# Kernel optimization log

Measured on AMD Instinct MI355X. Metric: run time of the kernel, lower is better.

The kernel has to match this reference:

```python
import jax, jax.numpy as jnp
import numpy as np

# hps: rnn_size=512, num_mixture=5, input_seq_width=35, output_seq_width=32,
#      batch_size=128, max_seq_len=1000
B, T, D_IN, Z, H, K = 128, 1000, 35, 32, 512, 5
OUT = 3 * K * Z  # 3 * num_mixture * output_seq_width = 480


def setup_inputs() -> dict:
    key = jax.random.key(0)
    ks = jax.random.split(key, 5)
    scale = 0.05
    return {
        "inputs": jax.random.normal(ks[0], (B, T, D_IN), jnp.float32),
        # Keras LSTMCell params: kernel [D,4H], recurrent_kernel [H,4H], bias [4H]
        # gate order: i, f, g(candidate), o
        "Wk": jax.random.normal(ks[1], (D_IN, 4 * H), jnp.float32) * scale,
        "Wr": jax.random.normal(ks[2], (H, 4 * H), jnp.float32) * scale,
        "b": jnp.zeros((4 * H,), jnp.float32),
        # MDN Dense head: [H, 3*K*Z]
        "Wd": jax.random.normal(ks[3], (H, OUT), jnp.float32) * scale,
        "bd": jnp.zeros((OUT,), jnp.float32),
    }


def reference(inputs, Wk, Wr, b, Wd, bd):
    # split into (vae_z, a) then concat back -> identity, kept for faithfulness
    vae_z, a = inputs[..., :Z], inputs[..., Z:]
    z_a = jnp.concatenate([vae_z, a], axis=2)  # [B, T, D_IN]

    # precompute input projection for all timesteps (hoisted out of the scan)
    xz = jnp.einsum('btd,dk->btk', z_a, Wk) + b  # [B, T, 4H]
    xz_t = jnp.swapaxes(xz, 0, 1)                # [T, B, 4H]

    h0 = jnp.zeros((z_a.shape[0], H), xz.dtype)

    def step(carry, xt):
        h, c = carry
        gates = xt + h @ Wr  # [B, 4H]
        i, f, g, o = jnp.split(gates, 4, axis=-1)
        c = jax.nn.sigmoid(f) * c + jax.nn.sigmoid(i) * jnp.tanh(g)
        h = jax.nn.sigmoid(o) * jnp.tanh(c)
        return (h, c), h

    _, hs = jax.lax.scan(step, (h0, h0), xz_t)   # hs: [T, B, H]
    rnn_out = jnp.swapaxes(hs, 0, 1).reshape(-1, H)  # [B*T, H]
    out = rnn_out @ Wd + bd  # [B*T, 3*K*Z] mu/logstd/logpi MDN params
    return out
```

## Files before the change

### kernel.cpp

```cpp
#include <hip/hip_runtime.h>


#define NGRP   8
#define NSLICE 32
#define GB     16
#define HH     512
#define TT     1000
#define DIN    35
#define OUTC   480
#define ODC    15
#define HWORDS 2048

typedef __bf16 bf16x8 __attribute__((ext_vector_type(8)));
typedef float  f32x4  __attribute__((ext_vector_type(4)));
typedef unsigned short u16;
typedef unsigned int   u32;
typedef unsigned long long u64;

__device__ __forceinline__ u16 f2bf(float x) {
    u32 u = __float_as_uint(x);
    u += 0x7FFFu + ((u >> 16) & 1u);
    return (u16)(u >> 16);
}
__device__ __forceinline__ float sigf(float x) { return 1.0f / (1.0f + __expf(-x)); }
__device__ __forceinline__ float tanh_fast(float x) {
    float ax = fabsf(x);
    float e = __expf(-2.0f * ax);
    return copysignf((1.0f - e) / (1.0f + e), x);
}
__device__ __forceinline__ u32 pk2f(float a, float b) {
    return (u32)f2bf(a) | ((u32)f2bf(b) << 16);
}

union bf8u { u32 u[4]; bf16x8 v; };

#define BARRIER() do { asm volatile("" ::: "memory"); \
                       __builtin_amdgcn_s_barrier(); \
                       asm volatile("" ::: "memory"); \
                       __builtin_amdgcn_sched_barrier(0); } while (0)
#define WAIT_LGKM() do { asm volatile("s_waitcnt lgkmcnt(0)" ::: "memory"); \
                         __builtin_amdgcn_sched_barrier(0); } while (0)
#define WAIT_VM()   do { asm volatile("s_waitcnt vmcnt(0)" ::: "memory"); \
                         __builtin_amdgcn_sched_barrier(0); } while (0)

#define MFMA16(a, b, c) __builtin_amdgcn_mfma_f32_16x16x32_bf16((a), (b), (c), 0, 0, 0)

__global__ void __launch_bounds__(512, 1)
mdn_kernel(const float* __restrict__ inp, const float* __restrict__ Wk,
           const float* __restrict__ Wr,  const float* __restrict__ bg,
           const float* __restrict__ Wd,  const float* __restrict__ bd,
           float* __restrict__ out, u32* __restrict__ flags, u64* __restrict__ hbuf)
{
    __shared__ __attribute__((aligned(16))) u16  wr_s[64 * HH];
    __shared__ __attribute__((aligned(16))) u16  wk_s[64 * 64];
    __shared__ __attribute__((aligned(16))) u16  wd_s[16 * HH];
    __shared__ __attribute__((aligned(16))) u16  h_s [GB * HH];
    __shared__ __attribute__((aligned(16))) float gbuf[4 * 256];
    __shared__ __attribute__((aligned(16))) float pbuf[2 * 4 * 256];

    const int tid  = threadIdx.x;
    const int lane = tid & 63;
    const int wave = tid >> 6;
    const int g    = blockIdx.x & 7;
    const int s    = blockIdx.x >> 3;
    const int m16  = lane & 15;
    const int kq   = lane >> 4;

    {
        int n = tid & 63;
        int q = n >> 4, j4 = n & 15;
        int col = q * HH + s * 16 + j4;
        for (int k = tid >> 6; k < HH; k += 8)
            wr_s[n * HH + (k ^ ((n & 7) << 3))] = f2bf(Wr[(size_t)k * 2048 + col]);
        for (int k = tid >> 6; k < 64; k += 8)
            wk_s[n * 64 + (k ^ ((n & 7) << 3))] = f2bf(k < DIN ? Wk[(size_t)k * 2048 + col] : 0.0f);
    }
    {
        int n = tid & 15;
        for (int k = tid >> 4; k < HH; k += 32)
            wd_s[n * HH + (k ^ ((n & 7) << 3))] =
                f2bf(n < ODC ? Wd[(size_t)k * OUTC + s * ODC + n] : 0.0f);
    }
    for (int i = tid; i < GB * HH / 4; i += 512) ((u64*)h_s)[i] = 0ull;
    __syncthreads();

    bf16x8 bfr[18];
    if (wave < 4) {
        int nloc = (m16 & 3) * 16 + 4 * wave + (m16 >> 2);
        #pragma unroll
        for (int ks = 0; ks < 16; ++ks) {
            int k0 = 32 * ks + 8 * kq;
            bfr[ks] = *(const bf16x8*)(&wr_s[nloc * HH + (k0 ^ ((nloc & 7) << 3))]);
        }
        #pragma unroll
        for (int i = 0; i < 2; ++i) {
            int k0 = 32 * i + 8 * kq;
            bfr[16 + i] = *(const bf16x8*)(&wk_s[nloc * 64 + (k0 ^ ((nloc & 7) << 3))]);
        }
    } else {
        int w4 = wave - 4;
        #pragma unroll
        for (int kk = 0; kk < 4; ++kk) {
            int k0 = w4 * 128 + 32 * kk + 8 * kq;
            bfr[kk] = *(const bf16x8*)(&wd_s[m16 * HH + (k0 ^ ((m16 & 7) << 3))]);
        }
    }

    float c_reg = 0.f;
    float bi = 0.f, bff = 0.f, bgg = 0.f, boo = 0.f, bdv = 0.f;
    const int cb = lane & 15;
    const int ce = lane >> 4;
    if (wave < 4) {
        int jj = 4 * wave + ce;
        int scol = s * 16 + jj;
        bi  = bg[0 * HH + scol];
        bff = bg[1 * HH + scol];
        bgg = bg[2 * HH + scol];
        boo = bg[3 * HH + scol];
    } else {
        int oo = lane & 15;
        if (oo < ODC) bdv = bd[s * ODC + oo];
    }

    float xr[8];
    float xe0 = 0.f, xe1 = 0.f, xe2 = 0.f;
    #pragma unroll
    for (int i = 0; i < 8; ++i) xr[i] = 0.f;
    if (wave < 4) {
        const float* ip = inp + ((size_t)(g * GB + m16) * TT + 0) * DIN;
        #pragma unroll
        for (int i = 0; i < 8; ++i) xr[i] = ip[kq * 8 + i];
        if (kq == 0) { xe0 = ip[32]; xe1 = ip[33]; xe2 = ip[34]; }
    }
    __syncthreads();

    const int pb = tid >> 5;
    const int pk = tid & 31;

    for (int t = 0; t <= TT + 1; ++t) {
        if (wave < 4) {
            if (t < TT) {
                bf8u a0, a1;
                a0.u[0] = pk2f(xr[0], xr[1]); a0.u[1] = pk2f(xr[2], xr[3]);
                a0.u[2] = pk2f(xr[4], xr[5]); a0.u[3] = pk2f(xr[6], xr[7]);
                a1.u[0] = (kq == 0) ? pk2f(xe0, xe1) : 0u;
                a1.u[1] = (kq == 0) ? pk2f(xe2, 0.f) : 0u;
                a1.u[2] = 0u; a1.u[3] = 0u;
                f32x4 acc0 = {0,0,0,0}, acc1 = {0,0,0,0};
                acc0 = MFMA16(a0.v, bfr[16], acc0);
                acc1 = MFMA16(a1.v, bfr[17], acc1);
                #pragma unroll
                for (int ks = 0; ks < 16; ks += 2) {
                    int k0 = 32 * ks + 8 * kq;
                    bf16x8 a = *(const bf16x8*)(&h_s[m16 * HH + (k0 ^ ((m16 & 7) << 3))]);
                    acc0 = MFMA16(a, bfr[ks], acc0);
                    int k1 = 32 * (ks + 1) + 8 * kq;
                    bf16x8 a2 = *(const bf16x8*)(&h_s[m16 * HH + (k1 ^ ((m16 & 7) << 3))]);
                    acc1 = MFMA16(a2, bfr[ks + 1], acc1);
                }
                #pragma unroll
                for (int j = 0; j < 4; ++j)
                    gbuf[wave * 256 + (kq * 4 + j) * 16 + m16] = acc0[j] + acc1[j];
                WAIT_LGKM();
                f32x4 gv = *(const f32x4*)(&gbuf[wave * 256 + cb * 16 + 4 * ce]);
                float iv = gv[0] + bi, fv = gv[1] + bff;
                float gg2 = gv[2] + bgg, ov = gv[3] + boo;
                c_reg = sigf(fv) * c_reg + sigf(iv) * tanh_fast(gg2);
                float h = sigf(ov) * tanh_fast(c_reg);
                u32 hb32 = (u32)f2bf(h);
                u32 o1 = (u32)__shfl_xor((int)hb32, 16);
                u32 pair = ((ce & 1) == 0) ? (hb32 | (o1 << 16)) : (o1 | (hb32 << 16));
                u32 o2 = (u32)__shfl_xor((int)pair, 32);
                if (ce == 0) {
                    u64 w64 = (u64)pair | ((u64)o2 << 32);
                    u64* dst = hbuf + (size_t)(t & 1) * (NGRP * HWORDS) + g * HWORDS
                                  + cb * 128 + s * 4 + wave;
                    __hip_atomic_store(dst, w64, __ATOMIC_RELAXED, __HIP_MEMORY_SCOPE_AGENT);
                }
                WAIT_VM();
                if (lane == 0)
                    __hip_atomic_store(&flags[(g * 128 + s * 4 + wave) * 16], (u32)(t + 1),
                                       __ATOMIC_RELAXED, __HIP_MEMORY_SCOPE_AGENT);
                if (t + 1 < TT) {
                    const float* ip = inp + ((size_t)(g * GB + m16) * TT + (t + 1)) * DIN;
                    #pragma unroll
                    for (int i = 0; i < 8; ++i) xr[i] = ip[kq * 8 + i];
                    if (kq == 0) { xe0 = ip[32]; xe1 = ip[33]; xe2 = ip[34]; }
                }
            }
        } else {
            int w4 = wave - 4;
            if (t >= 1 && t <= TT) {
                f32x4 acc0 = {0,0,0,0}, acc1 = {0,0,0,0};
                #pragma unroll
                for (int kk = 0; kk < 4; kk += 2) {
                    int k0 = w4 * 128 + 32 * kk + 8 * kq;
                    bf16x8 a = *(const bf16x8*)(&h_s[m16 * HH + (k0 ^ ((m16 & 7) << 3))]);
                    acc0 = MFMA16(a, bfr[kk], acc0);
                    int k1 = w4 * 128 + 32 * (kk + 1) + 8 * kq;
                    bf16x8 a2 = *(const bf16x8*)(&h_s[m16 * HH + (k1 ^ ((m16 & 7) << 3))]);
                    acc1 = MFMA16(a2, bfr[kk + 1], acc1);
                }
                #pragma unroll
                for (int j = 0; j < 4; ++j)
                    pbuf[(t & 1) * 1024 + w4 * 256 + (kq * 4 + j) * 16 + m16] = acc0[j] + acc1[j];
            }
            if (t >= 2) {
                int bb = 4 * w4 + (lane >> 4);
                int oo = lane & 15;
                int par = ((t & 1) ^ 1) * 1024;
                float v = pbuf[par + 0 * 256 + bb * 16 + oo]
                        + pbuf[par + 1 * 256 + bb * 16 + oo]
                        + pbuf[par + 2 * 256 + bb * 16 + oo]
                        + pbuf[par + 3 * 256 + bb * 16 + oo] + bdv;
                if (oo < ODC)
                    out[((size_t)(g * GB + bb) * TT + (t - 2)) * OUTC + s * ODC + oo] = v;
            }
        }

        if (t < TT) {
            if (wave == 0) {
                const u32* f0 = flags + (g * 128 + lane) * 16;
                const u32* f1 = flags + (g * 128 + 64 + lane) * 16;
                const u32 tgt = (u32)(t + 1);
                int spins = 0;
                while (true) {
                    u32 a = __hip_atomic_load(f0, __ATOMIC_RELAXED, __HIP_MEMORY_SCOPE_AGENT);
                    u32 b = __hip_atomic_load(f1, __ATOMIC_RELAXED, __HIP_MEMORY_SCOPE_AGENT);
                    if (__all((int)(a >= tgt && b >= tgt))) break;
                    __builtin_amdgcn_s_sleep(1);
                    if (++spins > (1 << 18)) break;
                }
            }
            BARRIER();
            {
                const u64* bp = hbuf + (size_t)(t & 1) * (NGRP * HWORDS) + g * HWORDS;
                #pragma unroll
                for (int i = 0; i < 2; ++i) {
                    int widx = pb * 128 + pk * 2 + i * 64;
                    u64 vlo = __hip_atomic_load(bp + widx,     __ATOMIC_RELAXED, __HIP_MEMORY_SCOPE_AGENT);
                    u64 vhi = __hip_atomic_load(bp + widx + 1, __ATOMIC_RELAXED, __HIP_MEMORY_SCOPE_AGENT);
                    int k  = pk * 8 + i * 256;
                    int sk = k ^ ((pb & 7) << 3);
                    *(u64*)(&h_s[pb * HH + sk])     = vlo;
                    *(u64*)(&h_s[pb * HH + sk + 4]) = vhi;
                }
            }
            WAIT_LGKM(); BARRIER();
        } else {
            WAIT_LGKM(); BARRIER();
        }
    }
}

extern "C" void kernel_launch(void* const* d_in, const int* in_sizes, int n_in,
                              void* d_out, int out_size, void* d_ws, size_t ws_size,
                              hipStream_t stream) {
    const float* inp = (const float*)d_in[0];
    const float* Wk  = (const float*)d_in[1];
    const float* Wr  = (const float*)d_in[2];
    const float* bg  = (const float*)d_in[3];
    const float* Wd  = (const float*)d_in[4];
    const float* bd  = (const float*)d_in[5];
    float* out = (float*)d_out;

    char* ws = (char*)d_ws;
    u32* flags = (u32*)ws;
    u64* hbuf  = (u64*)(ws + 65536);
    hipMemsetAsync(d_ws, 0, 65536, stream);

    hipLaunchKernelGGL(mdn_kernel, dim3(NGRP * NSLICE), dim3(512), 0, stream,
                       inp, Wk, Wr, bg, Wd, bd, out, flags, hbuf);
}
```

Before: 2.993 ms.

## Aggregate per-block publish flags via LDS counter and relayout h exchange buffer

Each block now counts its four compute waves' publishes in a shared LDS counter, and only the last wave writes a single per-block flag. This cuts the flags each group polls per step from 128 to 32, so one load per lane replaces two. The global h exchange layout changes so each wave writes contiguous words and every thread gathers four coalesced u64s into swizzled LDS. The output waves now store the previous step's result before the projection MFMAs. The risks are the extra LDS atomic on the critical path and a memory-ordering subtlety, since the flag store does not wait for the other waves' hbuf stores to complete.

```diff
diff --git a/kernel.cpp b/kernel.cpp
--- a/kernel.cpp
+++ b/kernel.cpp
@@ -57,6 +57,7 @@
     __shared__ __attribute__((aligned(16))) u16  h_s [GB * HH];
     __shared__ __attribute__((aligned(16))) float gbuf[4 * 256];
     __shared__ __attribute__((aligned(16))) float pbuf[2 * 4 * 256];
+    __shared__ int pubcnt;
 
     const int tid  = threadIdx.x;
     const int lane = tid & 63;
@@ -82,6 +83,7 @@
                 f2bf(n < ODC ? Wd[(size_t)k * OUTC + s * ODC + n] : 0.0f);
     }
     for (int i = tid; i < GB * HH / 4; i += 512) ((u64*)h_s)[i] = 0ull;
+    if (tid == 0) pubcnt = 0;
     __syncthreads();
 
     bf16x8 bfr[18];
@@ -133,9 +135,6 @@
         if (kq == 0) { xe0 = ip[32]; xe1 = ip[33]; xe2 = ip[34]; }
     }
     __syncthreads();
-
-    const int pb = tid >> 5;
-    const int pk = tid & 31;
 
     for (int t = 0; t <= TT + 1; ++t) {
         if (wave < 4) {
@@ -174,13 +173,16 @@
                 if (ce == 0) {
                     u64 w64 = (u64)pair | ((u64)o2 << 32);
                     u64* dst = hbuf + (size_t)(t & 1) * (NGRP * HWORDS) + g * HWORDS
-                                  + cb * 128 + s * 4 + wave;
+                                  + s * 64 + wave * 16 + cb;
                     __hip_atomic_store(dst, w64, __ATOMIC_RELAXED, __HIP_MEMORY_SCOPE_AGENT);
                 }
                 WAIT_VM();
-                if (lane == 0)
-                    __hip_atomic_store(&flags[(g * 128 + s * 4 + wave) * 16], (u32)(t + 1),
-                                       __ATOMIC_RELAXED, __HIP_MEMORY_SCOPE_AGENT);
+                if (lane == 0) {
+                    int old = atomicAdd(&pubcnt, 1);
+                    if (old == 4 * t + 3)
+                        __hip_atomic_store(&flags[(g * NSLICE + s) * 16], (u32)(t + 1),
+                                           __ATOMIC_RELAXED, __HIP_MEMORY_SCOPE_AGENT);
+                }
                 if (t + 1 < TT) {
                     const float* ip = inp + ((size_t)(g * GB + m16) * TT + (t + 1)) * DIN;
                     #pragma unroll
@@ -190,21 +192,6 @@
             }
         } else {
             int w4 = wave - 4;
-            if (t >= 1 && t <= TT) {
-                f32x4 acc0 = {0,0,0,0}, acc1 = {0,0,0,0};
-                #pragma unroll
-                for (int kk = 0; kk < 4; kk += 2) {
-                    int k0 = w4 * 128 + 32 * kk + 8 * kq;
-                    bf16x8 a = *(const bf16x8*)(&h_s[m16 * HH + (k0 ^ ((m16 & 7) << 3))]);
-                    acc0 = MFMA16(a, bfr[kk], acc0);
-                    int k1 = w4 * 128 + 32 * (kk + 1) + 8 * kq;
-                    bf16x8 a2 = *(const bf16x8*)(&h_s[m16 * HH + (k1 ^ ((m16 & 7) << 3))]);
-                    acc1 = MFMA16(a2, bfr[kk + 1], acc1);
-                }
-                #pragma unroll
-                for (int j = 0; j < 4; ++j)
-                    pbuf[(t & 1) * 1024 + w4 * 256 + (kq * 4 + j) * 16 + m16] = acc0[j] + acc1[j];
-            }
             if (t >= 2) {
                 int bb = 4 * w4 + (lane >> 4);
                 int oo = lane & 15;
@@ -216,34 +203,45 @@
                 if (oo < ODC)
                     out[((size_t)(g * GB + bb) * TT + (t - 2)) * OUTC + s * ODC + oo] = v;
             }
+            if (t >= 1 && t <= TT) {
+                f32x4 acc0 = {0,0,0,0}, acc1 = {0,0,0,0};
+                #pragma unroll
+                for (int kk = 0; kk < 4; kk += 2) {
+                    int k0 = w4 * 128 + 32 * kk + 8 * kq;
+                    bf16x8 a = *(const bf16x8*)(&h_s[m16 * HH + (k0 ^ ((m16 & 7) << 3))]);
+                    acc0 = MFMA16(a, bfr[kk], acc0);
+                    int k1 = w4 * 128 + 32 * (kk + 1) + 8 * kq;
+                    bf16x8 a2 = *(const bf16x8*)(&h_s[m16 * HH + (k1 ^ ((m16 & 7) << 3))]);
+                    acc1 = MFMA16(a2, bfr[kk + 1], acc1);
+                }
+                #pragma unroll
+                for (int j = 0; j < 4; ++j)
+                    pbuf[(t & 1) * 1024 + w4 * 256 + (kq * 4 + j) * 16 + m16] = acc0[j] + acc1[j];
+            }
         }
 
         if (t < TT) {
             if (wave == 0) {
-                const u32* f0 = flags + (g * 128 + lane) * 16;
-                const u32* f1 = flags + (g * 128 + 64 + lane) * 16;
+                const u32* fp = flags + (g * NSLICE + (lane & 31)) * 16;
                 const u32 tgt = (u32)(t + 1);
                 int spins = 0;
                 while (true) {
-                    u32 a = __hip_atomic_load(f0, __ATOMIC_RELAXED, __HIP_MEMORY_SCOPE_AGENT);
-                    u32 b = __hip_atomic_load(f1, __ATOMIC_RELAXED, __HIP_MEMORY_SCOPE_AGENT);
-                    if (__all((int)(a >= tgt && b >= tgt))) break;
+                    u32 v = __hip_atomic_load(fp, __ATOMIC_RELAXED, __HIP_MEMORY_SCOPE_AGENT);
+                    if (__all((int)(v >= tgt))) break;
                     __builtin_amdgcn_s_sleep(1);
-                    if (++spins > (1 << 18)) break;
+                    if (++spins > (1 << 20)) break;
                 }
             }
             BARRIER();
             {
                 const u64* bp = hbuf + (size_t)(t & 1) * (NGRP * HWORDS) + g * HWORDS;
                 #pragma unroll
-                for (int i = 0; i < 2; ++i) {
-                    int widx = pb * 128 + pk * 2 + i * 64;
-                    u64 vlo = __hip_atomic_load(bp + widx,     __ATOMIC_RELAXED, __HIP_MEMORY_SCOPE_AGENT);
-                    u64 vhi = __hip_atomic_load(bp + widx + 1, __ATOMIC_RELAXED, __HIP_MEMORY_SCOPE_AGENT);
-                    int k  = pk * 8 + i * 256;
-                    int sk = k ^ ((pb & 7) << 3);
-                    *(u64*)(&h_s[pb * HH + sk])     = vlo;
-                    *(u64*)(&h_s[pb * HH + sk + 4]) = vhi;
+                for (int i = 0; i < 4; ++i) {
+                    int L = tid + i * 512;
+                    u64 v = __hip_atomic_load(bp + L, __ATOMIC_RELAXED, __HIP_MEMORY_SCOPE_AGENT);
+                    int b    = L & 15;
+                    int kcol = (L >> 6) * 16 + 4 * ((L >> 4) & 3);
+                    *(u64*)(&h_s[b * HH + (kcol ^ ((b & 7) << 3))]) = v;
                 }
             }
             WAIT_LGKM(); BARRIER();
@@ -266,8 +264,8 @@
 
     char* ws = (char*)d_ws;
     u32* flags = (u32*)ws;
-    u64* hbuf  = (u64*)(ws + 65536);
-    hipMemsetAsync(d_ws, 0, 65536, stream);
+    u64* hbuf  = (u64*)(ws + 16384);
+    hipMemsetAsync(d_ws, 0, 16384, stream);
 
     hipLaunchKernelGGL(mdn_kernel, dim3(NGRP * NSLICE), dim3(512), 0, stream,
                        inp, Wk, Wr, bg, Wd, bd, out, flags, hbuf);
```

Result: no change. 2.941 ms (-1.7%).
